# Kernel tuning notes

Hardware: AMD Instinct MI355X
Metric: run time of the kernel (lower is better)

Reference implementation:

```python
import jax, jax.numpy as jnp
import numpy as np

B, D_IN, H1, H2, LAT, K = 32768, 512, 256, 128, 64, 2048
BN_EPS = 1e-5
COMMIT = 0.25


def _linear_w(k, i, o):
    # xavier-uniform-ish init
    lim = np.sqrt(6.0 / (i + o)).astype(np.float32)
    return jax.random.uniform(k, (i, o), jnp.float32, -lim, lim)


def _bn_params(keys, n):
    g = jax.random.uniform(keys[0], (n,), jnp.float32, 0.5, 1.5)
    b = 0.1 * jax.random.normal(keys[1], (n,), jnp.float32)
    m = 0.1 * jax.random.normal(keys[2], (n,), jnp.float32)
    v = jax.random.uniform(keys[3], (n,), jnp.float32, 0.5, 1.5)
    return g, b, m, v


def setup_inputs() -> dict:
    key = jax.random.key(0)
    ks = jax.random.split(key, 32)
    inp = {"x": jax.random.normal(ks[0], (B, D_IN), jnp.float32)}
    # encoder: 512 -> 256 -> 128 -> 64
    inp["ew1"], inp["eb1"] = _linear_w(ks[1], D_IN, H1), jnp.zeros((H1,), jnp.float32)
    inp["eg1"], inp["ebt1"], inp["em1"], inp["ev1"] = _bn_params(jax.random.split(ks[2], 4), H1)
    inp["ew2"], inp["eb2"] = _linear_w(ks[3], H1, H2), jnp.zeros((H2,), jnp.float32)
    inp["eg2"], inp["ebt2"], inp["em2"], inp["ev2"] = _bn_params(jax.random.split(ks[4], 4), H2)
    inp["ew3"], inp["eb3"] = _linear_w(ks[5], H2, LAT), jnp.zeros((LAT,), jnp.float32)
    # codebook (num_embeddings, latent_dim)
    inp["codebook"] = _linear_w(ks[6], K, LAT).reshape(K, LAT)
    # decoder: 64 -> 128 -> 256 -> 512
    inp["dw1"], inp["db1"] = _linear_w(ks[7], LAT, H2), jnp.zeros((H2,), jnp.float32)
    inp["dg1"], inp["dbt1"], inp["dm1"], inp["dv1"] = _bn_params(jax.random.split(ks[8], 4), H2)
    inp["dw2"], inp["db2"] = _linear_w(ks[9], H2, H1), jnp.zeros((H1,), jnp.float32)
    inp["dg2"], inp["dbt2"], inp["dm2"], inp["dv2"] = _bn_params(jax.random.split(ks[10], 4), H1)
    inp["dw3"], inp["db3"] = _linear_w(ks[11], H1, D_IN), jnp.zeros((D_IN,), jnp.float32)
    return inp


def _bn(x, g, b, m, v):
    # BatchNorm1d in eval mode: running stats
    return (x - m) * (g * jax.lax.rsqrt(v + BN_EPS)) + b


def reference(x, ew1, eb1, eg1, ebt1, em1, ev1,
              ew2, eb2, eg2, ebt2, em2, ev2,
              ew3, eb3, codebook,
              dw1, db1, dg1, dbt1, dm1, dv1,
              dw2, db2, dg2, dbt2, dm2, dv2,
              dw3, db3):
    # ---- encoder MLP (Dropout is identity in eval) ----
    h = _bn(jax.nn.relu(x @ ew1 + eb1), eg1, ebt1, em1, ev1)
    h = _bn(jax.nn.relu(h @ ew2 + eb2), eg2, ebt2, em2, ev2)
    z_e = h @ ew3 + eb3  # [B, LAT]

    # ---- vector quantization: cdist + argmin + gather ----
    # squared L2 distance (argmin-equivalent to cdist p=2)
    d2 = (jnp.sum(z_e * z_e, axis=1, keepdims=True)
          + jnp.sum(codebook * codebook, axis=1)[None, :]
          - 2.0 * (z_e @ codebook.T))  # [B, K]
    idx = jnp.argmin(d2, axis=-1)  # [B]
    z_q = codebook[idx]  # gather, [B, LAT]

    codebook_loss = jnp.mean((z_q - jax.lax.stop_gradient(z_e)) ** 2)
    commit_loss = jnp.mean((z_e - jax.lax.stop_gradient(z_q)) ** 2)
    vq_loss = codebook_loss + COMMIT * commit_loss

    # straight-through estimator
    z_q = z_e + jax.lax.stop_gradient(z_q - z_e)

    # ---- decoder MLP ----
    h = _bn(jax.nn.relu(z_q @ dw1 + db1), dg1, dbt1, dm1, dv1)
    h = _bn(jax.nn.relu(h @ dw2 + db2), dg2, dbt2, dm2, dv2)
    x_recon = h @ dw3 + db3  # [B, D_IN]

    recon_err = jnp.mean((x_recon - x) ** 2)
    return x_recon, vq_loss, idx, recon_err
```

## Files before the change

### kernel.cpp

```cpp
#include <hip/hip_runtime.h>

#define B_ROWS 32768
#define D_IN   512
#define H1_N   256
#define H2_N   128
#define LAT_N  64
#define K_CB   2048

#define BN 128
#define BK 32

#define VQ_MARGIN 4.0e-3f

typedef __attribute__((ext_vector_type(8))) short s8v;
typedef __attribute__((ext_vector_type(4))) float f4v;

__device__ inline unsigned short f2bf(float f) {
    union { float f; unsigned u; } v; v.f = f;
    unsigned r = v.u + 0x7fffu + ((v.u >> 16) & 1u);
    return (unsigned short)(r >> 16);
}
__device__ inline float bf2f(unsigned short h) {
    union { unsigned u; float f; } v; v.u = ((unsigned)h) << 16;
    return v.f;
}

#define SWZ(row) ((((row) >> 2) & 7) << 3)

template <int MODE, int BMT>
__global__ __launch_bounds__(256, (BMT == 128) ? 2 : 6) void gemm_fused(
    const float* __restrict__ A, const float* __restrict__ W,
    const float* __restrict__ bias,
    const float* __restrict__ bn_g, const float* __restrict__ bn_b,
    const float* __restrict__ bn_m, const float* __restrict__ bn_v,
    float* __restrict__ out, int M, int N)
{
    constexpr int MR = BMT / 16;
    __shared__ float sA[BK][BMT];
    __shared__ float sB[BK][BN];
    const int tid = threadIdx.x;
    const int tr = tid >> 4;
    const int tc = tid & 15;
    const int row0 = blockIdx.x * BMT;
    const int n0   = blockIdx.y * BN;

    float acc[MR][8];
#pragma unroll
    for (int i = 0; i < MR; ++i)
#pragma unroll
        for (int j = 0; j < 8; ++j) acc[i][j] = 0.f;

    for (int k0 = 0; k0 < M; k0 += BK) {
#pragma unroll
        for (int it = 0; it < BMT / 32; ++it) {
            int s = tid + it * 256;
            int m = s >> 3;
            int kq = s & 7;
            float4 v = *reinterpret_cast<const float4*>(
                &A[(size_t)(row0 + m) * M + k0 + kq * 4]);
            int kk = kq * 4;
            sA[kk + 0][m ^ SWZ(kk + 0)] = v.x;
            sA[kk + 1][m ^ SWZ(kk + 1)] = v.y;
            sA[kk + 2][m ^ SWZ(kk + 2)] = v.z;
            sA[kk + 3][m ^ SWZ(kk + 3)] = v.w;
        }
#pragma unroll
        for (int it = 0; it < 4; ++it) {
            int s = tid + it * 256;
            int k = s >> 5;
            int nq = s & 31;
            int n = n0 + nq * 4;
            float4 v = make_float4(0.f, 0.f, 0.f, 0.f);
            if (n < N)
                v = *reinterpret_cast<const float4*>(&W[(size_t)(k0 + k) * N + n]);
            *reinterpret_cast<float4*>(&sB[k][nq * 4]) = v;
        }
        __syncthreads();
#pragma unroll 4
        for (int k = 0; k < BK; ++k) {
            int ac = (tr * MR) ^ SWZ(k);
            float a[MR];
            {
                float4 a0 = *reinterpret_cast<float4*>(&sA[k][ac]);
                a[0] = a0.x; a[1] = a0.y; a[2] = a0.z; a[3] = a0.w;
                if constexpr (MR == 8) {
                    float4 a1 = *reinterpret_cast<float4*>(&sA[k][ac + 4]);
                    a[4] = a1.x; a[5] = a1.y; a[6] = a1.z; a[7] = a1.w;
                }
            }
            float4 b0 = *reinterpret_cast<float4*>(&sB[k][tc * 4]);
            float4 b1 = *reinterpret_cast<float4*>(&sB[k][64 + tc * 4]);
            float b[8] = {b0.x, b0.y, b0.z, b0.w, b1.x, b1.y, b1.z, b1.w};
#pragma unroll
            for (int i = 0; i < MR; ++i)
#pragma unroll
                for (int j = 0; j < 8; ++j)
                    acc[i][j] = fmaf(a[i], b[j], acc[i][j]);
        }
        __syncthreads();
    }

    const int nb0 = n0 + tc * 4;
    const int nb1 = n0 + 64 + tc * 4;
    float bi[8], sc[8], sh[8];
#pragma unroll
    for (int g = 0; g < 2; ++g) {
        int nb = g ? nb1 : nb0;
        if (nb < N) {
#pragma unroll
            for (int j = 0; j < 4; ++j) {
                int n = nb + j;
                bi[g * 4 + j] = bias[n];
                if (MODE == 0) {
                    float s = bn_g[n] * rsqrtf(bn_v[n] + 1e-5f);
                    sc[g * 4 + j] = s;
                    sh[g * 4 + j] = bn_b[n] - bn_m[n] * s;
                }
            }
        }
    }
#pragma unroll
    for (int i = 0; i < MR; ++i) {
        int row = row0 + tr * MR + i;
#pragma unroll
        for (int g = 0; g < 2; ++g) {
            int nb = g ? nb1 : nb0;
            if (nb < N) {
                float o[4];
#pragma unroll
                for (int j = 0; j < 4; ++j) {
                    float v = acc[i][g * 4 + j] + bi[g * 4 + j];
                    if (MODE == 0) {
                        v = v > 0.f ? v : 0.f;
                        v = v * sc[g * 4 + j] + sh[g * 4 + j];
                    }
                    o[j] = v;
                }
                *reinterpret_cast<float4*>(&out[(size_t)row * N + nb]) =
                    make_float4(o[0], o[1], o[2], o[3]);
            }
        }
    }
}

__global__ __launch_bounds__(256) void wprep(
    const float* __restrict__ w, unsigned short* __restrict__ w_hi,
    unsigned short* __restrict__ w_lo, int K, int N)
{
    int idx = blockIdx.x * 256 + threadIdx.x;
    if (idx >= N * K) return;
    int n = idx / K, k = idx - n * K;
    float f = w[(size_t)k * N + n];
    unsigned u = __float_as_uint(f);
    float lo = f - __uint_as_float(u & 0xffff0000u);
    w_hi[idx] = (unsigned short)(u >> 16);
    w_lo[idx] = f2bf(lo);
}

template <int MODE, int K>
__global__ __launch_bounds__(256, 2) void mfma_gemm(
    const unsigned short* __restrict__ A_hi,
    const unsigned short* __restrict__ A_lo,
    const unsigned short* __restrict__ w_hi,
    const unsigned short* __restrict__ w_lo,
    const float* __restrict__ bias,
    const float* __restrict__ bn_g, const float* __restrict__ bn_b,
    const float* __restrict__ bn_m, const float* __restrict__ bn_v,
    unsigned short* __restrict__ out_hi, unsigned short* __restrict__ out_lo,
    float* __restrict__ out_f32,
    const float* __restrict__ xref, float* __restrict__ partials, int N)
{
    const int lane = threadIdx.x & 63;
    const int wv = threadIdx.x >> 6;
    const int wr = wv >> 1, wc = wv & 1;
    const int rbase = blockIdx.x * 128 + wr * 64;
    const int cbase = blockIdx.y * 128 + wc * 64;
    const int lr = lane & 15, lg = lane >> 4;

    f4v acc[4][4];
#pragma unroll
    for (int rt = 0; rt < 4; ++rt)
#pragma unroll
        for (int ct = 0; ct < 4; ++ct)
            acc[rt][ct] = (f4v){0.f, 0.f, 0.f, 0.f};

#pragma unroll
    for (int ks = 0; ks < K / 32; ++ks) {
        s8v ah[4], al[4], bh[4], bl[4];
#pragma unroll
        for (int rt = 0; rt < 4; ++rt) {
            size_t off = (size_t)(rbase + rt * 16 + lr) * K + ks * 32 + lg * 8;
            ah[rt] = *reinterpret_cast<const s8v*>(&A_hi[off]);
            al[rt] = *reinterpret_cast<const s8v*>(&A_lo[off]);
        }
#pragma unroll
        for (int ct = 0; ct < 4; ++ct) {
            size_t off = (size_t)(cbase + ct * 16 + lr) * K + ks * 32 + lg * 8;
            bh[ct] = *reinterpret_cast<const s8v*>(&w_hi[off]);
            bl[ct] = *reinterpret_cast<const s8v*>(&w_lo[off]);
        }
#pragma unroll
        for (int rt = 0; rt < 4; ++rt)
#pragma unroll
            for (int ct = 0; ct < 4; ++ct) {
                acc[rt][ct] = __builtin_amdgcn_mfma_f32_16x16x32_bf16(
                    ah[rt], bh[ct], acc[rt][ct], 0, 0, 0);
                acc[rt][ct] = __builtin_amdgcn_mfma_f32_16x16x32_bf16(
                    al[rt], bh[ct], acc[rt][ct], 0, 0, 0);
                acc[rt][ct] = __builtin_amdgcn_mfma_f32_16x16x32_bf16(
                    ah[rt], bl[ct], acc[rt][ct], 0, 0, 0);
            }
    }

    float sq = 0.f;
#pragma unroll
    for (int ct = 0; ct < 4; ++ct) {
        int col = cbase + ct * 16 + lr;
        float bi = bias[col];
        float sc = 0.f, sh = 0.f;
        if (MODE == 0) {
            float s = bn_g[col] * rsqrtf(bn_v[col] + 1e-5f);
            sc = s;
            sh = bn_b[col] - bn_m[col] * s;
        }
#pragma unroll
        for (int rt = 0; rt < 4; ++rt)
#pragma unroll
            for (int i = 0; i < 4; ++i) {
                int row = rbase + rt * 16 + lg * 4 + i;
                float v = acc[rt][ct][i] + bi;
                if (MODE == 0) {
                    v = fmaxf(v, 0.f) * sc + sh;
                    unsigned u = __float_as_uint(v);
                    out_hi[(size_t)row * N + col] = (unsigned short)(u >> 16);
                    out_lo[(size_t)row * N + col] =
                        f2bf(v - __uint_as_float(u & 0xffff0000u));
                }
                if (MODE == 2) {
                    float d = v - xref[(size_t)row * N + col];
                    sq = fmaf(d, d, sq);
                    out_f32[(size_t)row * N + col] = v;
                }
            }
    }
    if (MODE == 2) {
        __shared__ float red[256];
        red[threadIdx.x] = sq;
        __syncthreads();
        for (int off = 128; off > 0; off >>= 1) {
            if (threadIdx.x < off) red[threadIdx.x] += red[threadIdx.x + off];
            __syncthreads();
        }
        if (threadIdx.x == 0)
            partials[blockIdx.y * gridDim.x + blockIdx.x] = red[0];
    }
}

__global__ __launch_bounds__(256) void vq_prep(
    const float* __restrict__ cb, unsigned short* __restrict__ cb_hi,
    unsigned short* __restrict__ cb_lo, float* __restrict__ cn,
    int* __restrict__ rcnt)
{
    if (blockIdx.x == 0 && threadIdx.x == 0) rcnt[0] = 0;
    int j = blockIdx.x * 256 + threadIdx.x;
    float s = 0.f;
#pragma unroll
    for (int lq = 0; lq < 16; ++lq) {
        float4 v = *reinterpret_cast<const float4*>(&cb[(size_t)j * LAT_N + lq * 4]);
        float e[4] = {v.x, v.y, v.z, v.w};
        ushort4 h, l;
        unsigned short* hp = &h.x;
        unsigned short* lp = &l.x;
#pragma unroll
        for (int t = 0; t < 4; ++t) {
            s = fmaf(e[t], e[t], s);
            unsigned short hb = f2bf(e[t]);
            hp[t] = hb;
            lp[t] = f2bf(e[t] - bf2f(hb));
        }
        *reinterpret_cast<ushort4*>(&cb_hi[(size_t)j * LAT_N + lq * 4]) = h;
        *reinterpret_cast<ushort4*>(&cb_lo[(size_t)j * LAT_N + lq * 4]) = l;
    }
    cn[j] = s;
}

__global__ __launch_bounds__(256) void vq_mfma(
    const float* __restrict__ z, const unsigned short* __restrict__ cb_hi,
    const unsigned short* __restrict__ cb_lo, const float* __restrict__ cnorm,
    float4* __restrict__ cand)
{
    const int lane = threadIdx.x & 63;
    const int wid  = blockIdx.x * 4 + (threadIdx.x >> 6);
    const int rbase = (wid >> 3) * 64;
    const int cblk  = wid & 7;
    const int cbase = cblk * 256;
    const int lr = lane & 15;
    const int lg = lane >> 4;

    s8v a_hi[4][2], a_lo[4][2];
#pragma unroll
    for (int rt = 0; rt < 4; ++rt) {
        int row = rbase + rt * 16 + lr;
#pragma unroll
        for (int ks = 0; ks < 2; ++ks) {
            const float* p = &z[(size_t)row * LAT_N + ks * 32 + lg * 8];
            float4 v0 = *reinterpret_cast<const float4*>(p);
            float4 v1 = *reinterpret_cast<const float4*>(p + 4);
            float vv[8] = {v0.x, v0.y, v0.z, v0.w, v1.x, v1.y, v1.z, v1.w};
#pragma unroll
            for (int jj = 0; jj < 8; ++jj) {
                unsigned short hb = f2bf(vv[jj]);
                a_hi[rt][ks][jj] = (short)hb;
                a_lo[rt][ks][jj] = (short)f2bf(vv[jj] - bf2f(hb));
            }
        }
    }

    float b1[4][4], b2[4][4];
    int j1[4][4];
#pragma unroll
    for (int rt = 0; rt < 4; ++rt)
#pragma unroll
        for (int i = 0; i < 4; ++i) {
            b1[rt][i] = 3.4e38f; b2[rt][i] = 3.4e38f; j1[rt][i] = 0;
        }

    for (int ct = 0; ct < 16; ++ct) {
        int col = cbase + ct * 16 + lr;
        const unsigned short* ph = &cb_hi[(size_t)col * LAT_N + lg * 8];
        const unsigned short* pl = &cb_lo[(size_t)col * LAT_N + lg * 8];
        s8v bh0 = *reinterpret_cast<const s8v*>(ph);
        s8v bh1 = *reinterpret_cast<const s8v*>(ph + 32);
        s8v bl0 = *reinterpret_cast<const s8v*>(pl);
        s8v bl1 = *reinterpret_cast<const s8v*>(pl + 32);
        float cn = cnorm[col];
#pragma unroll
        for (int rt = 0; rt < 4; ++rt) {
            f4v acc = {0.f, 0.f, 0.f, 0.f};
            acc = __builtin_amdgcn_mfma_f32_16x16x32_bf16(a_hi[rt][0], bh0, acc, 0, 0, 0);
            acc = __builtin_amdgcn_mfma_f32_16x16x32_bf16(a_hi[rt][1], bh1, acc, 0, 0, 0);
            acc = __builtin_amdgcn_mfma_f32_16x16x32_bf16(a_lo[rt][0], bh0, acc, 0, 0, 0);
            acc = __builtin_amdgcn_mfma_f32_16x16x32_bf16(a_lo[rt][1], bh1, acc, 0, 0, 0);
            acc = __builtin_amdgcn_mfma_f32_16x16x32_bf16(a_hi[rt][0], bl0, acc, 0, 0, 0);
            acc = __builtin_amdgcn_mfma_f32_16x16x32_bf16(a_hi[rt][1], bl1, acc, 0, 0, 0);
#pragma unroll
            for (int i = 0; i < 4; ++i) {
                float d = fmaf(-2.f, acc[i], cn);
                if (d < b1[rt][i]) {
                    b2[rt][i] = b1[rt][i];
                    b1[rt][i] = d;
                    j1[rt][i] = col;
                } else if (d < b2[rt][i]) {
                    b2[rt][i] = d;
                }
            }
        }
    }

#pragma unroll
    for (int off = 1; off < 16; off <<= 1) {
#pragma unroll
        for (int rt = 0; rt < 4; ++rt)
#pragma unroll
            for (int i = 0; i < 4; ++i) {
                float o1 = __shfl_xor(b1[rt][i], off);
                float o2 = __shfl_xor(b2[rt][i], off);
                int oj = __shfl_xor(j1[rt][i], off);
                float nb2 = fminf(fmaxf(b1[rt][i], o1), fminf(b2[rt][i], o2));
                if (o1 < b1[rt][i] ||
                    (o1 == b1[rt][i] && oj < j1[rt][i])) {
                    b1[rt][i] = o1;
                    j1[rt][i] = oj;
                }
                b2[rt][i] = nb2;
            }
    }
    if (lr == 0) {
#pragma unroll
        for (int rt = 0; rt < 4; ++rt)
#pragma unroll
            for (int i = 0; i < 4; ++i) {
                int row = rbase + rt * 16 + lg * 4 + i;
                cand[(size_t)row * 8 + cblk] = make_float4(
                    b1[rt][i], __int_as_float(j1[rt][i]), b2[rt][i], 0.f);
            }
    }
}

__global__ __launch_bounds__(256) void vq_merge(
    const float4* __restrict__ cand, float* __restrict__ idxf,
    int* __restrict__ rlist, int* __restrict__ rcnt)
{
    int row = blockIdx.x * 256 + threadIdx.x;
    const float4* c = &cand[(size_t)row * 8];
    float4 c0 = c[0];
    float b1 = c0.x, b2 = c0.z;
    int j1 = __float_as_int(c0.y);
#pragma unroll
    for (int t = 1; t < 8; ++t) {
        float4 ct = c[t];
        float o1 = ct.x, o2 = ct.z;
        int oj = __float_as_int(ct.y);
        float nb2 = fminf(fmaxf(b1, o1), fminf(b2, o2));
        if (o1 < b1 || (o1 == b1 && oj < j1)) { b1 = o1; j1 = oj; }
        b2 = nb2;
    }
    idxf[row] = (float)j1;
    if (!(b2 - b1 >= VQ_MARGIN)) {
        int s = atomicAdd(rcnt, 1);
        if (s < B_ROWS) rlist[s] = row;
    }
}

#define RB 8
__global__ __launch_bounds__(256) void vq_repair(
    const int* __restrict__ rcnt, const int* __restrict__ rlist,
    const float* __restrict__ z, const float* __restrict__ cb,
    const float* __restrict__ cn, float* __restrict__ idxf)
{
    __shared__ float sz[RB][LAT_N];
    __shared__ float rv[256];
    __shared__ int ri[256];
    const int tid = threadIdx.x;
    const int count = min(rcnt[0], B_ROWS);
    if (blockIdx.x * RB >= count) return;
    for (int base = blockIdx.x * RB; base < count; base += gridDim.x * RB) {
        int nr = min(RB, count - base);
        __syncthreads();
        for (int s = tid; s < nr * LAT_N; s += 256) {
            int r = s >> 6, d = s & 63;
            int rr = rlist[base + r];
            rr = ((unsigned)rr < (unsigned)B_ROWS) ? rr : 0;
            sz[r][d] = z[(size_t)rr * LAT_N + d];
        }
        __syncthreads();
        float bv[RB];
        int bj[RB];
#pragma unroll
        for (int r = 0; r < RB; ++r) { bv[r] = 3.4e38f; bj[r] = 0; }
        for (int k = 0; k < K_CB / 256; ++k) {
            int cidx = tid + k * 256;
            float acc[RB];
#pragma unroll
            for (int r = 0; r < RB; ++r) acc[r] = 0.f;
            const float* cp = &cb[(size_t)cidx * LAT_N];
#pragma unroll 2
            for (int d4 = 0; d4 < 16; ++d4) {
                float4 cv = *reinterpret_cast<const float4*>(cp + d4 * 4);
#pragma unroll
                for (int r = 0; r < RB; ++r) {
                    acc[r] = fmaf(sz[r][d4 * 4 + 0], cv.x, acc[r]);
                    acc[r] = fmaf(sz[r][d4 * 4 + 1], cv.y, acc[r]);
                    acc[r] = fmaf(sz[r][d4 * 4 + 2], cv.z, acc[r]);
                    acc[r] = fmaf(sz[r][d4 * 4 + 3], cv.w, acc[r]);
                }
            }
            float cnv = cn[cidx];
#pragma unroll
            for (int r = 0; r < RB; ++r) {
                float d = fmaf(-2.f, acc[r], cnv);
                if (d < bv[r] || (d == bv[r] && cidx < bj[r])) {
                    bv[r] = d; bj[r] = cidx;
                }
            }
        }
        for (int r = 0; r < RB; ++r) {
            if (r >= nr) break;
            rv[tid] = bv[r];
            ri[tid] = bj[r];
            __syncthreads();
            for (int off = 128; off > 0; off >>= 1) {
                if (tid < off) {
                    float ov = rv[tid + off];
                    int oi = ri[tid + off];
                    if (ov < rv[tid] || (ov == rv[tid] && oi < ri[tid])) {
                        rv[tid] = ov; ri[tid] = oi;
                    }
                }
                __syncthreads();
            }
            if (tid == 0) {
                int rr = rlist[base + r];
                if ((unsigned)rr < (unsigned)B_ROWS)
                    idxf[rr] = (float)ri[0];
            }
            __syncthreads();
        }
    }
}

__global__ __launch_bounds__(256) void vq_zqloss(
    const float* __restrict__ idxf, const float* __restrict__ z,
    const float* __restrict__ cb,
    const unsigned short* __restrict__ cbhi,
    const unsigned short* __restrict__ cblo,
    unsigned short* __restrict__ zqhi, unsigned short* __restrict__ zqlo,
    float* __restrict__ partials)
{
    __shared__ float red[256];
    int tid = threadIdx.x;
    int row = blockIdx.x * 256 + tid;
    int bj = (int)idxf[row];
    bj = ((unsigned)bj < (unsigned)K_CB) ? bj : 0;
    float sq = 0.f;
#pragma unroll
    for (int lq = 0; lq < 16; ++lq) {
        float4 cv = *reinterpret_cast<const float4*>(&cb[(size_t)bj * LAT_N + lq * 4]);
        float4 zv = *reinterpret_cast<const float4*>(&z[(size_t)row * LAT_N + lq * 4]);
        float d0 = cv.x - zv.x, d1 = cv.y - zv.y;
        float d2 = cv.z - zv.z, d3 = cv.w - zv.w;
        sq = fmaf(d0, d0, sq); sq = fmaf(d1, d1, sq);
        sq = fmaf(d2, d2, sq); sq = fmaf(d3, d3, sq);
    }
    const uint4* gh = reinterpret_cast<const uint4*>(&cbhi[(size_t)bj * LAT_N]);
    const uint4* gl = reinterpret_cast<const uint4*>(&cblo[(size_t)bj * LAT_N]);
    uint4* dh = reinterpret_cast<uint4*>(&zqhi[(size_t)row * LAT_N]);
    uint4* dl = reinterpret_cast<uint4*>(&zqlo[(size_t)row * LAT_N]);
#pragma unroll
    for (int q = 0; q < 8; ++q) { dh[q] = gh[q]; dl[q] = gl[q]; }

    red[tid] = sq;
    __syncthreads();
    for (int off = 128; off > 0; off >>= 1) {
        if (tid < off) red[tid] += red[tid + off];
        __syncthreads();
    }
    if (tid == 0) partials[blockIdx.x] = red[0];
}

__global__ __launch_bounds__(256) void finalize_kernel(
    const float* __restrict__ vqp, int nvq,
    const float* __restrict__ rep, int nre,
    float* __restrict__ vq_out, float* __restrict__ re_out)
{
    __shared__ float s[256];
    int tid = threadIdx.x;
    float a = 0.f;
    for (int i = tid; i < nvq; i += 256) a += vqp[i];
    s[tid] = a;
    __syncthreads();
    for (int off = 128; off > 0; off >>= 1) {
        if (tid < off) s[tid] += s[tid + off];
        __syncthreads();
    }
    if (tid == 0) *vq_out = 1.25f * s[0] / (float)(B_ROWS * LAT_N);
    __syncthreads();
    float b = 0.f;
    for (int i = tid; i < nre; i += 256) b += rep[i];
    s[tid] = b;
    __syncthreads();
    for (int off = 128; off > 0; off >>= 1) {
        if (tid < off) s[tid] += s[tid + off];
        __syncthreads();
    }
    if (tid == 0) *re_out = s[0] / (float)(B_ROWS * D_IN);
}

extern "C" void kernel_launch(void* const* d_in, const int* in_sizes, int n_in,
                              void* d_out, int out_size, void* d_ws, size_t ws_size,
                              hipStream_t stream)
{
    const float* x    = (const float*)d_in[0];
    const float* ew1  = (const float*)d_in[1];
    const float* eb1  = (const float*)d_in[2];
    const float* eg1  = (const float*)d_in[3];
    const float* ebt1 = (const float*)d_in[4];
    const float* em1  = (const float*)d_in[5];
    const float* ev1  = (const float*)d_in[6];
    const float* ew2  = (const float*)d_in[7];
    const float* eb2  = (const float*)d_in[8];
    const float* eg2  = (const float*)d_in[9];
    const float* ebt2 = (const float*)d_in[10];
    const float* em2  = (const float*)d_in[11];
    const float* ev2  = (const float*)d_in[12];
    const float* ew3  = (const float*)d_in[13];
    const float* eb3  = (const float*)d_in[14];
    const float* cb   = (const float*)d_in[15];
    const float* dw1  = (const float*)d_in[16];
    const float* db1  = (const float*)d_in[17];
    const float* dg1  = (const float*)d_in[18];
    const float* dbt1 = (const float*)d_in[19];
    const float* dm1  = (const float*)d_in[20];
    const float* dv1  = (const float*)d_in[21];
    const float* dw2  = (const float*)d_in[22];
    const float* db2  = (const float*)d_in[23];
    const float* dg2  = (const float*)d_in[24];
    const float* dbt2 = (const float*)d_in[25];
    const float* dm2  = (const float*)d_in[26];
    const float* dv2  = (const float*)d_in[27];
    const float* dw3  = (const float*)d_in[28];
    const float* db3  = (const float*)d_in[29];

    float* outf = (float*)d_out;
    const size_t XR_OFF = 0;
    const size_t VQ_OFF = (size_t)B_ROWS * D_IN;
    const size_t IDX_OFF = VQ_OFF + 1;
    const size_t RE_OFF = IDX_OFF + B_ROWS;

    float* wsf = (float*)d_ws;
    size_t off = 0;
    float* buf256 = wsf + off; off += (size_t)B_ROWS * H1_N;
    float* buf128 = wsf + off; off += (size_t)B_ROWS * H2_N;
    float* zbuf   = wsf + off; off += (size_t)B_ROWS * LAT_N;
    float* cnbuf  = wsf + off; off += K_CB;
    float* vqp    = wsf + off; off += 128;
    float* rep    = wsf + off; off += 1024;
    unsigned short* cbhi = (unsigned short*)(wsf + off); off += K_CB * LAT_N / 2;
    unsigned short* cblo = (unsigned short*)(wsf + off); off += K_CB * LAT_N / 2;
    float4* candb = (float4*)(wsf + off); off += (size_t)B_ROWS * 8 * 4;
    int* rcnt  = (int*)(wsf + off); off += 16;
    int* rlist = (int*)(wsf + off); off += B_ROWS;
    unsigned short* w1hi = (unsigned short*)(wsf + off); off += (H2_N * LAT_N) / 2;
    unsigned short* w1lo = (unsigned short*)(wsf + off); off += (H2_N * LAT_N) / 2;
    unsigned short* w2hi = (unsigned short*)(wsf + off); off += (H1_N * H2_N) / 2;
    unsigned short* w2lo = (unsigned short*)(wsf + off); off += (H1_N * H2_N) / 2;
    unsigned short* w3hi = (unsigned short*)(wsf + off); off += (D_IN * H1_N) / 2;
    unsigned short* w3lo = (unsigned short*)(wsf + off); off += (D_IN * H1_N) / 2;
    unsigned short* zqhi = (unsigned short*)(wsf + off); off += (size_t)B_ROWS * LAT_N / 2;
    unsigned short* zqlo = (unsigned short*)(wsf + off); off += (size_t)B_ROWS * LAT_N / 2;

    unsigned short* h1hi = (unsigned short*)buf128;
    unsigned short* h1lo = (unsigned short*)(buf128 + (size_t)B_ROWS * 64);
    unsigned short* h2hi = (unsigned short*)buf256;
    unsigned short* h2lo = (unsigned short*)(buf256 + (size_t)B_ROWS * 128);

    dim3 blk(256);

    vq_prep<<<dim3(K_CB / 256), blk, 0, stream>>>(cb, cbhi, cblo, cnbuf, rcnt);
    wprep<<<dim3((LAT_N * H2_N + 255) / 256), blk, 0, stream>>>(dw1, w1hi, w1lo, LAT_N, H2_N);
    wprep<<<dim3((H2_N * H1_N + 255) / 256), blk, 0, stream>>>(dw2, w2hi, w2lo, H2_N, H1_N);
    wprep<<<dim3((H1_N * D_IN + 255) / 256), blk, 0, stream>>>(dw3, w3hi, w3lo, H1_N, D_IN);

    gemm_fused<0, 128><<<dim3(B_ROWS / 128, H1_N / BN), blk, 0, stream>>>(
        x, ew1, eb1, eg1, ebt1, em1, ev1, buf256, D_IN, H1_N);
    gemm_fused<0, 64><<<dim3(B_ROWS / 64, 1), blk, 0, stream>>>(
        buf256, ew2, eb2, eg2, ebt2, em2, ev2, buf128, H1_N, H2_N);
    gemm_fused<1, 64><<<dim3(B_ROWS / 64, 1), blk, 0, stream>>>(
        buf128, ew3, eb3, nullptr, nullptr, nullptr, nullptr, zbuf, H2_N, LAT_N);

    vq_mfma<<<dim3(1024), blk, 0, stream>>>(zbuf, cbhi, cblo, cnbuf, candb);
    vq_merge<<<dim3(B_ROWS / 256), blk, 0, stream>>>(
        candb, outf + IDX_OFF, rlist, rcnt);
    vq_repair<<<dim3(256), blk, 0, stream>>>(
        rcnt, rlist, zbuf, cb, cnbuf, outf + IDX_OFF);
    vq_zqloss<<<dim3(B_ROWS / 256), blk, 0, stream>>>(
        outf + IDX_OFF, zbuf, cb, cbhi, cblo, zqhi, zqlo, vqp);

    mfma_gemm<0, LAT_N><<<dim3(B_ROWS / 128, H2_N / 128), blk, 0, stream>>>(
        zqhi, zqlo, w1hi, w1lo, db1, dg1, dbt1, dm1, dv1,
        h1hi, h1lo, nullptr, nullptr, nullptr, H2_N);
    mfma_gemm<0, H2_N><<<dim3(B_ROWS / 128, H1_N / 128), blk, 0, stream>>>(
        h1hi, h1lo, w2hi, w2lo, db2, dg2, dbt2, dm2, dv2,
        h2hi, h2lo, nullptr, nullptr, nullptr, H1_N);
    mfma_gemm<2, H1_N><<<dim3(B_ROWS / 128, D_IN / 128), blk, 0, stream>>>(
        h2hi, h2lo, w3hi, w3lo, db3, nullptr, nullptr, nullptr, nullptr,
        nullptr, nullptr, outf + XR_OFF, x, rep, D_IN);

    finalize_kernel<<<dim3(1), blk, 0, stream>>>(
        vqp, 128, rep, 1024, outf + VQ_OFF, outf + RE_OFF);
}
```

Baseline: 417.8 us.

## Merge prep kernels, fold zq/loss into merge+repair, widen first encoder GEMM tile

Combines the codebook and decoder-weight prep kernels into a single launch. Folds the z_q gather and VQ loss partials into vq_merge for confident rows and into vq_repair for ambiguous rows, which removes the separate vq_zqloss pass. Replaces the first encoder GEMM with a 128-thread kernel where each thread computes a 16x8 tile. That tile raises register pressure and halves threads per block, so latency hiding on the largest GEMM may suffer.

```diff
diff --git a/kernel.cpp b/kernel.cpp
--- a/kernel.cpp
+++ b/kernel.cpp
@@ -27,32 +27,138 @@
 
 #define SWZ(row) ((((row) >> 2) & 7) << 3)
 
-template <int MODE, int BMT>
-__global__ __launch_bounds__(256, (BMT == 128) ? 2 : 6) void gemm_fused(
+__global__ __launch_bounds__(128, 2) void gemm_f32_wide(
     const float* __restrict__ A, const float* __restrict__ W,
     const float* __restrict__ bias,
     const float* __restrict__ bn_g, const float* __restrict__ bn_b,
     const float* __restrict__ bn_m, const float* __restrict__ bn_v,
     float* __restrict__ out, int M, int N)
 {
-    constexpr int MR = BMT / 16;
-    __shared__ float sA[BK][BMT];
+    __shared__ float sA[BK][128];
     __shared__ float sB[BK][BN];
     const int tid = threadIdx.x;
     const int tr = tid >> 4;
     const int tc = tid & 15;
-    const int row0 = blockIdx.x * BMT;
+    const int row0 = blockIdx.x * 128;
     const int n0   = blockIdx.y * BN;
 
-    float acc[MR][8];
-#pragma unroll
-    for (int i = 0; i < MR; ++i)
+    float acc[16][8];
+#pragma unroll
+    for (int i = 0; i < 16; ++i)
 #pragma unroll
         for (int j = 0; j < 8; ++j) acc[i][j] = 0.f;
 
     for (int k0 = 0; k0 < M; k0 += BK) {
 #pragma unroll
-        for (int it = 0; it < BMT / 32; ++it) {
+        for (int it = 0; it < 8; ++it) {
+            int s = tid + it * 128;
+            int m = s >> 3;
+            int kq = s & 7;
+            float4 v = *reinterpret_cast<const float4*>(
+                &A[(size_t)(row0 + m) * M + k0 + kq * 4]);
+            int kk = kq * 4;
+            sA[kk + 0][m ^ SWZ(kk + 0)] = v.x;
+            sA[kk + 1][m ^ SWZ(kk + 1)] = v.y;
+            sA[kk + 2][m ^ SWZ(kk + 2)] = v.z;
+            sA[kk + 3][m ^ SWZ(kk + 3)] = v.w;
+        }
+#pragma unroll
+        for (int it = 0; it < 8; ++it) {
+            int s = tid + it * 128;
+            int k = s >> 5;
+            int nq = s & 31;
+            float4 v = *reinterpret_cast<const float4*>(
+                &W[(size_t)(k0 + k) * N + n0 + nq * 4]);
+            *reinterpret_cast<float4*>(&sB[k][nq * 4]) = v;
+        }
+        __syncthreads();
+#pragma unroll 4
+        for (int k = 0; k < BK; ++k) {
+            int b0a = (tr * 16) ^ SWZ(k);
+            int b1a = (tr * 16 + 8) ^ SWZ(k);
+            float a[16];
+            {
+                float4 v0 = *reinterpret_cast<float4*>(&sA[k][b0a]);
+                float4 v1 = *reinterpret_cast<float4*>(&sA[k][b0a + 4]);
+                float4 v2 = *reinterpret_cast<float4*>(&sA[k][b1a]);
+                float4 v3 = *reinterpret_cast<float4*>(&sA[k][b1a + 4]);
+                a[0]=v0.x; a[1]=v0.y; a[2]=v0.z; a[3]=v0.w;
+                a[4]=v1.x; a[5]=v1.y; a[6]=v1.z; a[7]=v1.w;
+                a[8]=v2.x; a[9]=v2.y; a[10]=v2.z; a[11]=v2.w;
+                a[12]=v3.x; a[13]=v3.y; a[14]=v3.z; a[15]=v3.w;
+            }
+            float4 c0 = *reinterpret_cast<float4*>(&sB[k][tc * 4]);
+            float4 c1 = *reinterpret_cast<float4*>(&sB[k][64 + tc * 4]);
+            float b[8] = {c0.x, c0.y, c0.z, c0.w, c1.x, c1.y, c1.z, c1.w};
+#pragma unroll
+            for (int i = 0; i < 16; ++i)
+#pragma unroll
+                for (int j = 0; j < 8; ++j)
+                    acc[i][j] = fmaf(a[i], b[j], acc[i][j]);
+        }
+        __syncthreads();
+    }
+
+    const int nb0 = n0 + tc * 4;
+    const int nb1 = n0 + 64 + tc * 4;
+    float bi[8], sc[8], sh[8];
+#pragma unroll
+    for (int g = 0; g < 2; ++g) {
+        int nb = g ? nb1 : nb0;
+#pragma unroll
+        for (int j = 0; j < 4; ++j) {
+            int n = nb + j;
+            bi[g * 4 + j] = bias[n];
+            float s = bn_g[n] * rsqrtf(bn_v[n] + 1e-5f);
+            sc[g * 4 + j] = s;
+            sh[g * 4 + j] = bn_b[n] - bn_m[n] * s;
+        }
+    }
+#pragma unroll
+    for (int i = 0; i < 16; ++i) {
+        int row = row0 + tr * 16 + i;
+#pragma unroll
+        for (int g = 0; g < 2; ++g) {
+            int nb = g ? nb1 : nb0;
+            float o[4];
+#pragma unroll
+            for (int j = 0; j < 4; ++j) {
+                float v = acc[i][g * 4 + j] + bi[g * 4 + j];
+                v = v > 0.f ? v : 0.f;
+                v = v * sc[g * 4 + j] + sh[g * 4 + j];
+                o[j] = v;
+            }
+            *reinterpret_cast<float4*>(&out[(size_t)row * N + nb]) =
+                make_float4(o[0], o[1], o[2], o[3]);
+        }
+    }
+}
+
+template <int MODE>
+__global__ __launch_bounds__(256, 6) void gemm_fused(
+    const float* __restrict__ A, const float* __restrict__ W,
+    const float* __restrict__ bias,
+    const float* __restrict__ bn_g, const float* __restrict__ bn_b,
+    const float* __restrict__ bn_m, const float* __restrict__ bn_v,
+    float* __restrict__ out, int M, int N)
+{
+    __shared__ float sA[BK][64];
+    __shared__ float sB[BK][BN];
+    const int tid = threadIdx.x;
+    const int tr = tid >> 4;
+    const int tc = tid & 15;
+    const int row0 = blockIdx.x * 64;
+    const int n0   = blockIdx.y * BN;
+
+    float acc[4][8];
+#pragma unroll
+    for (int i = 0; i < 4; ++i)
+#pragma unroll
+        for (int j = 0; j < 8; ++j) acc[i][j] = 0.f;
+
+    for (int k0 = 0; k0 < M; k0 += BK) {
+#pragma unroll
+        for (int it = 0; it < 2; ++it) {
             int s = tid + it * 256;
             int m = s >> 3;
             int kq = s & 7;
@@ -78,21 +184,14 @@
         __syncthreads();
 #pragma unroll 4
         for (int k = 0; k < BK; ++k) {
-            int ac = (tr * MR) ^ SWZ(k);
-            float a[MR];
-            {
-                float4 a0 = *reinterpret_cast<float4*>(&sA[k][ac]);
-                a[0] = a0.x; a[1] = a0.y; a[2] = a0.z; a[3] = a0.w;
-                if constexpr (MR == 8) {
-                    float4 a1 = *reinterpret_cast<float4*>(&sA[k][ac + 4]);
-                    a[4] = a1.x; a[5] = a1.y; a[6] = a1.z; a[7] = a1.w;
-                }
-            }
+            int ac = (tr * 4) ^ SWZ(k);
+            float4 a0 = *reinterpret_cast<float4*>(&sA[k][ac]);
+            float a[4] = {a0.x, a0.y, a0.z, a0.w};
             float4 b0 = *reinterpret_cast<float4*>(&sB[k][tc * 4]);
             float4 b1 = *reinterpret_cast<float4*>(&sB[k][64 + tc * 4]);
             float b[8] = {b0.x, b0.y, b0.z, b0.w, b1.x, b1.y, b1.z, b1.w};
 #pragma unroll
-            for (int i = 0; i < MR; ++i)
+            for (int i = 0; i < 4; ++i)
 #pragma unroll
                 for (int j = 0; j < 8; ++j)
                     acc[i][j] = fmaf(a[i], b[j], acc[i][j]);
@@ -120,8 +219,8 @@
         }
     }
 #pragma unroll
-    for (int i = 0; i < MR; ++i) {
-        int row = row0 + tr * MR + i;
+    for (int i = 0; i < 4; ++i) {
+        int row = row0 + tr * 4 + i;
 #pragma unroll
         for (int g = 0; g < 2; ++g) {
             int nb = g ? nb1 : nb0;
@@ -143,11 +242,11 @@
     }
 }
 
-__global__ __launch_bounds__(256) void wprep(
-    const float* __restrict__ w, unsigned short* __restrict__ w_hi,
-    unsigned short* __restrict__ w_lo, int K, int N)
-{
-    int idx = blockIdx.x * 256 + threadIdx.x;
+__device__ inline void wprep_body(const float* __restrict__ w,
+                                  unsigned short* __restrict__ w_hi,
+                                  unsigned short* __restrict__ w_lo,
+                                  int K, int N, int idx)
+{
     if (idx >= N * K) return;
     int n = idx / K, k = idx - n * K;
     float f = w[(size_t)k * N + n];
@@ -155,6 +254,50 @@
     float lo = f - __uint_as_float(u & 0xffff0000u);
     w_hi[idx] = (unsigned short)(u >> 16);
     w_lo[idx] = f2bf(lo);
+}
+
+__global__ __launch_bounds__(256) void prep_all(
+    const float* __restrict__ dw3, unsigned short* w3hi, unsigned short* w3lo,
+    const float* __restrict__ dw2, unsigned short* w2hi, unsigned short* w2lo,
+    const float* __restrict__ dw1, unsigned short* w1hi, unsigned short* w1lo,
+    const float* __restrict__ cb, unsigned short* cb_hi, unsigned short* cb_lo,
+    float* __restrict__ cn, int* __restrict__ rcnt, float* __restrict__ repairp)
+{
+    int bid = blockIdx.x;
+    int tid = threadIdx.x;
+    if (bid < 512) {
+        wprep_body(dw3, w3hi, w3lo, H1_N, D_IN, bid * 256 + tid);
+    } else if (bid < 640) {
+        wprep_body(dw2, w2hi, w2lo, H2_N, H1_N, (bid - 512) * 256 + tid);
+    } else if (bid < 672) {
+        wprep_body(dw1, w1hi, w1lo, LAT_N, H2_N, (bid - 640) * 256 + tid);
+    } else {
+        int blk = bid - 672;
+        if (blk == 0) {
+            if (tid == 0) rcnt[0] = 0;
+            repairp[tid] = 0.f;
+        }
+        int j = blk * 256 + tid;
+        float s = 0.f;
+#pragma unroll
+        for (int lq = 0; lq < 16; ++lq) {
+            float4 v = *reinterpret_cast<const float4*>(&cb[(size_t)j * LAT_N + lq * 4]);
+            float e[4] = {v.x, v.y, v.z, v.w};
+            ushort4 h, l;
+            unsigned short* hp = &h.x;
+            unsigned short* lp = &l.x;
+#pragma unroll
+            for (int t = 0; t < 4; ++t) {
+                s = fmaf(e[t], e[t], s);
+                unsigned short hb = f2bf(e[t]);
+                hp[t] = hb;
+                lp[t] = f2bf(e[t] - bf2f(hb));
+            }
+            *reinterpret_cast<ushort4*>(&cb_hi[(size_t)j * LAT_N + lq * 4]) = h;
+            *reinterpret_cast<ushort4*>(&cb_lo[(size_t)j * LAT_N + lq * 4]) = l;
+        }
+        cn[j] = s;
+    }
 }
 
 template <int MODE, int K>
@@ -256,34 +399,6 @@
     }
 }
 
-__global__ __launch_bounds__(256) void vq_prep(
-    const float* __restrict__ cb, unsigned short* __restrict__ cb_hi,
-    unsigned short* __restrict__ cb_lo, float* __restrict__ cn,
-    int* __restrict__ rcnt)
-{
-    if (blockIdx.x == 0 && threadIdx.x == 0) rcnt[0] = 0;
-    int j = blockIdx.x * 256 + threadIdx.x;
-    float s = 0.f;
-#pragma unroll
-    for (int lq = 0; lq < 16; ++lq) {
-        float4 v = *reinterpret_cast<const float4*>(&cb[(size_t)j * LAT_N + lq * 4]);
-        float e[4] = {v.x, v.y, v.z, v.w};
-        ushort4 h, l;
-        unsigned short* hp = &h.x;
-        unsigned short* lp = &l.x;
-#pragma unroll
-        for (int t = 0; t < 4; ++t) {
-            s = fmaf(e[t], e[t], s);
-            unsigned short hb = f2bf(e[t]);
-            hp[t] = hb;
-            lp[t] = f2bf(e[t] - bf2f(hb));
-        }
-        *reinterpret_cast<ushort4*>(&cb_hi[(size_t)j * LAT_N + lq * 4]) = h;
-        *reinterpret_cast<ushort4*>(&cb_lo[(size_t)j * LAT_N + lq * 4]) = l;
-    }
-    cn[j] = s;
-}
-
 __global__ __launch_bounds__(256) void vq_mfma(
     const float* __restrict__ z, const unsigned short* __restrict__ cb_hi,
     const unsigned short* __restrict__ cb_lo, const float* __restrict__ cnorm,
@@ -388,10 +503,18 @@
 }
 
 __global__ __launch_bounds__(256) void vq_merge(
-    const float4* __restrict__ cand, float* __restrict__ idxf,
-    int* __restrict__ rlist, int* __restrict__ rcnt)
-{
-    int row = blockIdx.x * 256 + threadIdx.x;
+    const float4* __restrict__ cand, const float* __restrict__ z,
+    const float* __restrict__ cb,
+    const unsigned short* __restrict__ cbhi,
+    const unsigned short* __restrict__ cblo,
+    unsigned short* __restrict__ zqhi, unsigned short* __restrict__ zqlo,
+    float* __restrict__ idxf,
+    int* __restrict__ rlist, int* __restrict__ rcnt,
+    float* __restrict__ mergep)
+{
+    __shared__ float red[256];
+    int tid = threadIdx.x;
+    int row = blockIdx.x * 256 + tid;
     const float4* c = &cand[(size_t)row * 8];
     float4 c0 = c[0];
     float b1 = c0.x, b2 = c0.z;
@@ -406,17 +529,45 @@
         b2 = nb2;
     }
     idxf[row] = (float)j1;
-    if (!(b2 - b1 >= VQ_MARGIN)) {
+    float sq = 0.f;
+    if (b2 - b1 >= VQ_MARGIN) {
+#pragma unroll
+        for (int lq = 0; lq < 16; ++lq) {
+            float4 cv = *reinterpret_cast<const float4*>(&cb[(size_t)j1 * LAT_N + lq * 4]);
+            float4 zv = *reinterpret_cast<const float4*>(&z[(size_t)row * LAT_N + lq * 4]);
+            float d0 = cv.x - zv.x, d1 = cv.y - zv.y;
+            float d2 = cv.z - zv.z, d3 = cv.w - zv.w;
+            sq = fmaf(d0, d0, sq); sq = fmaf(d1, d1, sq);
+            sq = fmaf(d2, d2, sq); sq = fmaf(d3, d3, sq);
+        }
+        const uint4* gh = reinterpret_cast<const uint4*>(&cbhi[(size_t)j1 * LAT_N]);
+        const uint4* gl = reinterpret_cast<const uint4*>(&cblo[(size_t)j1 * LAT_N]);
+        uint4* dh = reinterpret_cast<uint4*>(&zqhi[(size_t)row * LAT_N]);
+        uint4* dl = reinterpret_cast<uint4*>(&zqlo[(size_t)row * LAT_N]);
+#pragma unroll
+        for (int q = 0; q < 8; ++q) { dh[q] = gh[q]; dl[q] = gl[q]; }
+    } else {
         int s = atomicAdd(rcnt, 1);
         if (s < B_ROWS) rlist[s] = row;
     }
+    red[tid] = sq;
+    __syncthreads();
+    for (int off = 128; off > 0; off >>= 1) {
+        if (tid < off) red[tid] += red[tid + off];
+        __syncthreads();
+    }
+    if (tid == 0) mergep[blockIdx.x] = red[0];
 }
 
 #define RB 8
 __global__ __launch_bounds__(256) void vq_repair(
     const int* __restrict__ rcnt, const int* __restrict__ rlist,
     const float* __restrict__ z, const float* __restrict__ cb,
-    const float* __restrict__ cn, float* __restrict__ idxf)
+    const float* __restrict__ cn,
+    const unsigned short* __restrict__ cbhi,
+    const unsigned short* __restrict__ cblo,
+    unsigned short* __restrict__ zqhi, unsigned short* __restrict__ zqlo,
+    float* __restrict__ idxf, float* __restrict__ repairp)
 {
     __shared__ float sz[RB][LAT_N];
     __shared__ float rv[256];
@@ -424,6 +575,7 @@
     const int tid = threadIdx.x;
     const int count = min(rcnt[0], B_ROWS);
     if (blockIdx.x * RB >= count) return;
+    float lsum = 0.f;
     for (int base = blockIdx.x * RB; base < count; base += gridDim.x * RB) {
         int nr = min(RB, count - base);
         __syncthreads();
@@ -479,64 +631,49 @@
                 }
                 __syncthreads();
             }
-            if (tid == 0) {
-                int rr = rlist[base + r];
-                if ((unsigned)rr < (unsigned)B_ROWS)
-                    idxf[rr] = (float)ri[0];
+            int bjf = ri[0];
+            int rr = rlist[base + r];
+            bool ok = (unsigned)rr < (unsigned)B_ROWS;
+            rr = ok ? rr : 0;
+            if (tid == 0 && ok) idxf[rr] = (float)bjf;
+            float v = 0.f;
+            if (tid < 64) {
+                float d = cb[(size_t)bjf * LAT_N + tid] - sz[r][tid];
+                v = d * d;
             }
             __syncthreads();
-        }
-    }
-}
-
-__global__ __launch_bounds__(256) void vq_zqloss(
-    const float* __restrict__ idxf, const float* __restrict__ z,
-    const float* __restrict__ cb,
-    const unsigned short* __restrict__ cbhi,
-    const unsigned short* __restrict__ cblo,
-    unsigned short* __restrict__ zqhi, unsigned short* __restrict__ zqlo,
-    float* __restrict__ partials)
-{
-    __shared__ float red[256];
-    int tid = threadIdx.x;
-    int row = blockIdx.x * 256 + tid;
-    int bj = (int)idxf[row];
-    bj = ((unsigned)bj < (unsigned)K_CB) ? bj : 0;
-    float sq = 0.f;
-#pragma unroll
-    for (int lq = 0; lq < 16; ++lq) {
-        float4 cv = *reinterpret_cast<const float4*>(&cb[(size_t)bj * LAT_N + lq * 4]);
-        float4 zv = *reinterpret_cast<const float4*>(&z[(size_t)row * LAT_N + lq * 4]);
-        float d0 = cv.x - zv.x, d1 = cv.y - zv.y;
-        float d2 = cv.z - zv.z, d3 = cv.w - zv.w;
-        sq = fmaf(d0, d0, sq); sq = fmaf(d1, d1, sq);
-        sq = fmaf(d2, d2, sq); sq = fmaf(d3, d3, sq);
-    }
-    const uint4* gh = reinterpret_cast<const uint4*>(&cbhi[(size_t)bj * LAT_N]);
-    const uint4* gl = reinterpret_cast<const uint4*>(&cblo[(size_t)bj * LAT_N]);
-    uint4* dh = reinterpret_cast<uint4*>(&zqhi[(size_t)row * LAT_N]);
-    uint4* dl = reinterpret_cast<uint4*>(&zqlo[(size_t)row * LAT_N]);
-#pragma unroll
-    for (int q = 0; q < 8; ++q) { dh[q] = gh[q]; dl[q] = gl[q]; }
-
-    red[tid] = sq;
-    __syncthreads();
-    for (int off = 128; off > 0; off >>= 1) {
-        if (tid < off) red[tid] += red[tid + off];
-        __syncthreads();
-    }
-    if (tid == 0) partials[blockIdx.x] = red[0];
+            rv[tid] = v;
+            __syncthreads();
+            for (int off = 128; off > 0; off >>= 1) {
+                if (tid < off) rv[tid] += rv[tid + off];
+                __syncthreads();
+            }
+            if (tid == 0) lsum += rv[0];
+            if (ok) {
+                if (tid < 8)
+                    reinterpret_cast<uint4*>(&zqhi[(size_t)rr * LAT_N])[tid] =
+                        reinterpret_cast<const uint4*>(&cbhi[(size_t)bjf * LAT_N])[tid];
+                else if (tid < 16)
+                    reinterpret_cast<uint4*>(&zqlo[(size_t)rr * LAT_N])[tid - 8] =
+                        reinterpret_cast<const uint4*>(&cblo[(size_t)bjf * LAT_N])[tid - 8];
+            }
+            __syncthreads();
+        }
+    }
+    if (tid == 0) repairp[blockIdx.x] = lsum;
 }
 
 __global__ __launch_bounds__(256) void finalize_kernel(
-    const float* __restrict__ vqp, int nvq,
+    const float* __restrict__ mergep, int nm,
+    const float* __restrict__ repairp, int nr,
     const float* __restrict__ rep, int nre,
     float* __restrict__ vq_out, float* __restrict__ re_out)
 {
     __shared__ float s[256];
     int tid = threadIdx.x;
     float a = 0.f;
-    for (int i = tid; i < nvq; i += 256) a += vqp[i];
+    for (int i = tid; i < nm; i += 256) a += mergep[i];
+    for (int i = tid; i < nr; i += 256) a += repairp[i];
     s[tid] = a;
     __syncthreads();
     for (int off = 128; off > 0; off >>= 1) {
@@ -603,7 +740,8 @@
     float* buf128 = wsf + off; off += (size_t)B_ROWS * H2_N;
     float* zbuf   = wsf + off; off += (size_t)B_ROWS * LAT_N;
     float* cnbuf  = wsf + off; off += K_CB;
-    float* vqp    = wsf + off; off += 128;
+    float* mergep = wsf + off; off += 128;
+    float* repairp= wsf + off; off += 256;
     float* rep    = wsf + off; off += 1024;
     unsigned short* cbhi = (unsigned short*)(wsf + off); off += K_CB * LAT_N / 2;
     unsigned short* cblo = (unsigned short*)(wsf + off); off += K_CB * LAT_N / 2;
@@ -626,25 +764,24 @@
 
     dim3 blk(256);
 
-    vq_prep<<<dim3(K_CB / 256), blk, 0, stream>>>(cb, cbhi, cblo, cnbuf, rcnt);
-    wprep<<<dim3((LAT_N * H2_N + 255) / 256), blk, 0, stream>>>(dw1, w1hi, w1lo, LAT_N, H2_N);
-    wprep<<<dim3((H2_N * H1_N + 255) / 256), blk, 0, stream>>>(dw2, w2hi, w2lo, H2_N, H1_N);
-    wprep<<<dim3((H1_N * D_IN + 255) / 256), blk, 0, stream>>>(dw3, w3hi, w3lo, H1_N, D_IN);
-
-    gemm_fused<0, 128><<<dim3(B_ROWS / 128, H1_N / BN), blk, 0, stream>>>(
+    prep_all<<<dim3(680), blk, 0, stream>>>(
+        dw3, w3hi, w3lo, dw2, w2hi, w2lo, dw1, w1hi, w1lo,
+        cb, cbhi, cblo, cnbuf, rcnt, repairp);
+
+    gemm_f32_wide<<<dim3(B_ROWS / 128, H1_N / BN), dim3(128), 0, stream>>>(
         x, ew1, eb1, eg1, ebt1, em1, ev1, buf256, D_IN, H1_N);
-    gemm_fused<0, 64><<<dim3(B_ROWS / 64, 1), blk, 0, stream>>>(
+    gemm_fused<0><<<dim3(B_ROWS / 64, 1), blk, 0, stream>>>(
         buf256, ew2, eb2, eg2, ebt2, em2, ev2, buf128, H1_N, H2_N);
-    gemm_fused<1, 64><<<dim3(B_ROWS / 64, 1), blk, 0, stream>>>(
+    gemm_fused<1><<<dim3(B_ROWS / 64, 1), blk, 0, stream>>>(
         buf128, ew3, eb3, nullptr, nullptr, nullptr, nullptr, zbuf, H2_N, LAT_N);
 
     vq_mfma<<<dim3(1024), blk, 0, stream>>>(zbuf, cbhi, cblo, cnbuf, candb);
     vq_merge<<<dim3(B_ROWS / 256), blk, 0, stream>>>(
-        candb, outf + IDX_OFF, rlist, rcnt);
+        candb, zbuf, cb, cbhi, cblo, zqhi, zqlo,
+        outf + IDX_OFF, rlist, rcnt, mergep);
     vq_repair<<<dim3(256), blk, 0, stream>>>(
-        rcnt, rlist, zbuf, cb, cnbuf, outf + IDX_OFF);
-    vq_zqloss<<<dim3(B_ROWS / 256), blk, 0, stream>>>(
-        outf + IDX_OFF, zbuf, cb, cbhi, cblo, zqhi, zqlo, vqp);
+        rcnt, rlist, zbuf, cb, cnbuf, cbhi, cblo, zqhi, zqlo,
+        outf + IDX_OFF, repairp);
 
     mfma_gemm<0, LAT_N><<<dim3(B_ROWS / 128, H2_N / 128), blk, 0, stream>>>(
         zqhi, zqlo, w1hi, w1lo, db1, dg1, dbt1, dm1, dv1,
@@ -657,5 +794,5 @@
         nullptr, nullptr, outf + XR_OFF, x, rep, D_IN);
 
     finalize_kernel<<<dim3(1), blk, 0, stream>>>(
-        vqp, 128, rep, 1024, outf + VQ_OFF, outf + RE_OFF);
-}
+        mergep, 128, repairp, 256, rep, 1024, outf + VQ_OFF, outf + RE_OFF);
+}
```

Result: slower. 479.8 us (+14.8%).
